# Performance work log

Measured on AMD Instinct MI355X. Metric: run time of the kernel, lower is better.

The kernel has to match this reference:

```python
import jax, jax.numpy as jnp
import numpy as np

N = 8192          # num atoms
K = 32            # neighbors per atom (init kwarg k)
CUTOFF = 10.0     # init kwarg cutoff
NUM_MOLS = 128


def setup_inputs() -> dict:
    key = jax.random.key(0)
    k1, k2 = jax.random.split(key)
    pos = jax.random.normal(k1, (N, 3), dtype=jnp.float32)
    batch = jnp.sort(jax.random.randint(k2, (N,), 0, NUM_MOLS)).astype(jnp.int32)
    return {"pos": pos, "batch": batch}


def _pairwise_dist(pos):
    # ||x_i - x_j|| via the gram-matrix expansion; avoids an [N,N,3] intermediate.
    sq_norm = jnp.sum(pos * pos, axis=-1)                     # [N]
    sq = sq_norm[:, None] + sq_norm[None, :] - 2.0 * (pos @ pos.T)  # [N,N]
    sq = jnp.maximum(sq, 0.0)
    # safe sqrt: exact 0 on the diagonal without nan-producing sqrt'(0) in grads
    safe = jnp.where(sq > 0, sq, 1.0)
    return jnp.where(sq > 0, jnp.sqrt(safe), 0.0)


def reference(pos, batch):
    n = pos.shape[0]
    pdist = _pairwise_dist(pos)                               # [N,N]
    rows = jnp.arange(n)
    diag = rows[:, None] == rows[None, :]
    cross = batch[:, None] != batch[None, :]
    outer = pdist > CUTOFF
    mask = diag | cross | outer
    pdist = jnp.where(mask, CUTOFF, pdist)
    neg_w, indices = jax.lax.top_k(-pdist, K)                 # [N,K] each
    rows_e = jnp.broadcast_to(rows[:, None], indices.shape)
    edge_index = jnp.stack([indices.reshape(-1), rows_e.reshape(-1)])  # [2, N*K]
    edge_weight = -neg_w.reshape(-1)                          # [N*K]
    return edge_index, edge_weight
```

## Files before the change

### kernel.cpp

```cpp
#include <hip/hip_runtime.h>


#define CUTOFF_F 10.0f
#define ROWS_PER_BLOCK 4

__device__ __forceinline__ float readlane_f(float v, int lane) {
    return __int_as_float(__builtin_amdgcn_readlane(__float_as_int(v), lane));
}
__device__ __forceinline__ int readlane_i(int v, int lane) {
    return __builtin_amdgcn_readlane(v, lane);
}
__device__ __forceinline__ unsigned long long shfl_xor_u64(unsigned long long x, int m) {
    const int lo = __shfl_xor((int)(unsigned)(x & 0xffffffffull), m, 64);
    const int hi = __shfl_xor((int)(unsigned)(x >> 32), m, 64);
    return ((unsigned long long)(unsigned)hi << 32) | (unsigned)lo;
}

__device__ __forceinline__ float dist_v(float4 pr, float4 pc, bool diag) {
    if (diag) return CUTOFF_F;
    float dot = __fadd_rn(__fadd_rn(__fmul_rn(pr.x, pc.x), __fmul_rn(pr.y, pc.y)),
                          __fmul_rn(pr.z, pc.z));
    float sq = __fsub_rn(__fadd_rn(pr.w, pc.w), __fadd_rn(dot, dot));
    sq = fmaxf(sq, 0.0f);
    float d = (sq > 0.0f) ? __fsqrt_rn(sq) : 0.0f;
    return (d > CUTOFF_F) ? CUTOFF_F : d;
}

__device__ __forceinline__ float4 load_pos4(const float* __restrict__ pos, int g) {
    float x = pos[g * 3 + 0];
    float y = pos[g * 3 + 1];
    float z = pos[g * 3 + 2];
    float sq = __fadd_rn(__fadd_rn(__fmul_rn(x, x), __fmul_rn(y, y)), __fmul_rn(z, z));
    return make_float4(x, y, z, sq);
}

__device__ __forceinline__ unsigned long long pack_key(float v, int c) {
    return ((unsigned long long)(unsigned)__float_as_int(v) << 32) | (unsigned)c;
}

__device__ __forceinline__ unsigned long long bitonic64(unsigned long long key, int lane) {
#pragma unroll
    for (int k = 2; k <= 64; k <<= 1) {
#pragma unroll
        for (int j = k >> 1; j > 0; j >>= 1) {
            const unsigned long long pk = shfl_xor_u64(key, j);
            const bool take_min = (((lane & j) == 0) == ((lane & k) == 0));
            key = ((pk < key) == take_min) ? pk : key;
        }
    }
    return key;
}

__device__ __forceinline__ void bitonic128(unsigned long long& ka,
                                           unsigned long long& kb, int lane) {
#pragma unroll
    for (int k = 2; k <= 128; k <<= 1) {
#pragma unroll
        for (int j = k >> 1; j > 0; j >>= 1) {
            if (j == 64) {
                const bool alt = ka < kb;
                const unsigned long long mn = alt ? ka : kb;
                const unsigned long long mx = alt ? kb : ka;
                ka = mn; kb = mx;
            } else {
                const unsigned long long pa = shfl_xor_u64(ka, j);
                const unsigned long long pb = shfl_xor_u64(kb, j);
                const bool low = ((lane & j) == 0);
                const bool upA = ((lane & k) == 0);
                const bool upB = (k == 64) ? false : upA;
                ka = ((pa < ka) == (low == upA)) ? pa : ka;
                kb = ((pb < kb) == (low == upB)) ? pb : kb;
            }
        }
    }
}

template <int NCH>
__device__ __forceinline__ void do_fill(const float* v, int m, int K, int lane,
                                        int start, int end, int n, int r, int NK,
                                        float* __restrict__ out) {
    const int mm = n - m;
    for (int fb = 0; fb < K - m; fb += 64) {
        const int t = fb + lane;
        const bool active = t < (K - m);
        int idx = 0;
        bool found = false;
        if (active) {
            if (t < start)            { idx = t;                      found = true; }
            else if (t - start >= mm) { idx = end + (t - start - mm); found = true; }
        }
        if (__any(active && !found)) {
            int cnt = 0;
#pragma unroll
            for (int jj = 0; jj < NCH; ++jj) {
                const int base = 64 * jj;
                const int lim  = min(n - base, 64);
                for (int cc = 0; cc < lim; ++cc) {
                    if (readlane_f(v[jj], cc) == CUTOFF_F) {
                        if (active && !found && cnt == t - start) {
                            idx = start + base + cc; found = true;
                        }
                        ++cnt;
                    }
                }
            }
        }
        if (active) {
            const int o = r * K + m + t;
            out[o]          = (float)idx;
            out[2 * NK + o] = CUTOFF_F;
        }
    }
}

__device__ __forceinline__ void row_core_sort64(const float* __restrict__ pos,
                                                float4 pr, int n, int lane,
                                                int start, int end, int r,
                                                float* __restrict__ out,
                                                int NK, int K) {
    const int c = lane;
    float v[1];
    v[0] = (c < n) ? dist_v(pr, load_pos4(pos, start + c), (start + c) == r)
                   : CUTOFF_F;
    unsigned long long key = pack_key(v[0], c);
    key = bitonic64(key, lane);

    const float vs = __int_as_float((int)(unsigned)(key >> 32));
    const int   cs = (int)(unsigned)(key & 0xffffffffull);
    if (lane < K && vs < CUTOFF_F) {
        const int o = r * K + lane;
        out[o]          = (float)(start + cs);
        out[2 * NK + o] = vs;
    }
    for (int k2 = lane; k2 < K; k2 += 64)
        out[NK + r * K + k2] = (float)r;
    const int m = __popcll(__ballot(v[0] < CUTOFF_F));
    if (m < K) do_fill<1>(v, m, K, lane, start, end, n, r, NK, out);
}

__device__ __forceinline__ void row_core_sort128(const float* __restrict__ pos,
                                                 float4 pr, int n, int lane,
                                                 int start, int end, int r,
                                                 float* __restrict__ out,
                                                 int NK, int K) {
    const int cA = lane, cB = 64 + lane;
    float v[2];
    v[0] = (cA < n) ? dist_v(pr, load_pos4(pos, start + cA), (start + cA) == r)
                    : CUTOFF_F;
    v[1] = (cB < n) ? dist_v(pr, load_pos4(pos, start + cB), (start + cB) == r)
                    : CUTOFF_F;
    unsigned long long ka = pack_key(v[0], cA);
    unsigned long long kb = pack_key(v[1], cB);
    bitonic128(ka, kb, lane);

    const float vsa = __int_as_float((int)(unsigned)(ka >> 32));
    const int   csa = (int)(unsigned)(ka & 0xffffffffull);
    if (lane < K && vsa < CUTOFF_F) {
        const int o = r * K + lane;
        out[o]          = (float)(start + csa);
        out[2 * NK + o] = vsa;
    }
    if (64 + lane < K) {
        const float vsb = __int_as_float((int)(unsigned)(kb >> 32));
        const int   csb = (int)(unsigned)(kb & 0xffffffffull);
        if (vsb < CUTOFF_F) {
            const int o = r * K + 64 + lane;
            out[o]          = (float)(start + csb);
            out[2 * NK + o] = vsb;
        }
    }
    for (int k2 = lane; k2 < K; k2 += 64)
        out[NK + r * K + k2] = (float)r;
    const int m = __popcll(__ballot(v[0] < CUTOFF_F))
                + __popcll(__ballot(v[1] < CUTOFF_F));
    if (m < K) do_fill<2>(v, m, K, lane, start, end, n, r, NK, out);
}

__device__ __attribute__((noinline))
int lower_bound_cold(const int* __restrict__ batch, int lo, int hi, int key) {
    while (lo < hi) {
        int mid = (lo + hi) >> 1;
        if (batch[mid] < key) lo = mid + 1; else hi = mid;
    }
    return lo;
}

__device__ __attribute__((noinline))
void row_core_fallback(const float* __restrict__ pos, float4 pr, int n, int lane,
                       int start, int end, int r, float* __restrict__ out,
                       int NK, int K) {
    int m = 0;
    for (int cb = 0; cb < n; cb += 64) {
        const int c = cb + lane;
        const float v = (c < n)
            ? dist_v(pr, load_pos4(pos, start + c), (start + c) == r) : CUTOFF_F;
        int rk = 0;
        for (int cc = 0; cc < n; ++cc) {
            const float vv = dist_v(pr, load_pos4(pos, start + cc), (start + cc) == r);
            rk += (vv < v) || (vv == v && cc < c);
        }
        if (c < n && v < CUTOFF_F && rk < K) {
            const int o = r * K + rk;
            out[o]          = (float)(start + c);
            out[2 * NK + o] = v;
        }
        m += __popcll(__ballot(c < n && v < CUTOFF_F));
    }
    for (int k2 = lane; k2 < K; k2 += 64)
        out[NK + r * K + k2] = (float)r;
    if (m < K) {
        const int mm = n - m;
        for (int fb = 0; fb < K - m; fb += 64) {
            const int t = fb + lane;
            const bool active = t < (K - m);
            int idx = 0; bool found = false;
            if (active) {
                if (t < start)            { idx = t;                      found = true; }
                else if (t - start >= mm) { idx = end + (t - start - mm); found = true; }
            }
            if (__any(active && !found)) {
                int cnt = 0;
                for (int cc = 0; cc < n; ++cc) {
                    if (dist_v(pr, load_pos4(pos, start + cc), (start + cc) == r)
                        == CUTOFF_F) {
                        if (active && !found && cnt == t - start) {
                            idx = start + cc; found = true;
                        }
                        ++cnt;
                    }
                }
            }
            if (active) {
                const int o = r * K + m + t;
                out[o]          = (float)idx;
                out[2 * NK + o] = CUTOFF_F;
            }
        }
    }
}

__global__ __launch_bounds__(256, 8)
void knn_fused_kernel(const float* __restrict__ pos,
                      const int* __restrict__ batch,
                      float* __restrict__ out,
                      int N, int K) {
    const int w    = threadIdx.x >> 6;
    const int lane = threadIdx.x & 63;
    const int r    = blockIdx.x * ROWS_PER_BLOCK + w;
    if (r >= N) return;
    const int NK = N * K;

    const int iu = r - 63 + lane;
    const int id = r + 1 + lane;
    const int au = batch[max(iu, 0)];
    const int ad = batch[min(id, N - 1)];
    const float4 pr = load_pos4(pos, r);

    const int b = readlane_i(au, 63);

    const unsigned long long mu = __ballot(iu >= 0 && au == b);
    int start;
    if (mu != ~0ull) {
        start = r - __builtin_clzll(~mu) + 1;
    } else {
        const int iu2 = r - 127 + lane;
        const unsigned long long mu2 =
            __ballot(iu2 >= 0 && batch[max(iu2, 0)] == b);
        if (mu2 != ~0ull)           start = r - 63 - __builtin_clzll(~mu2);
        else if (r - 127 <= 0)      start = 0;
        else                        start = lower_bound_cold(batch, 0, r, b);
    }

    const unsigned long long md = __ballot(id < N && ad == b);
    int end;
    if (md != ~0ull) {
        end = r + 1 + __builtin_ctzll(~md);
    } else {
        const int id2 = r + 65 + lane;
        const unsigned long long md2 =
            __ballot(id2 < N && batch[min(id2, N - 1)] == b);
        if (md2 != ~0ull)           end = r + 65 + __builtin_ctzll(~md2);
        else if (r + 129 >= N)      end = N;
        else                        end = lower_bound_cold(batch, r + 1, N, b + 1);
    }

    const int n = end - start;

    if      (n <= 64)  row_core_sort64 (pos, pr, n, lane, start, end, r, out, NK, K);
    else if (n <= 128) row_core_sort128(pos, pr, n, lane, start, end, r, out, NK, K);
    else               row_core_fallback(pos, pr, n, lane, start, end, r, out, NK, K);
}

extern "C" void kernel_launch(void* const* d_in, const int* in_sizes, int n_in,
                              void* d_out, int out_size, void* d_ws, size_t ws_size,
                              hipStream_t stream) {
    const float* pos   = (const float*)d_in[0];
    const int*   batch = (const int*)d_in[1];
    float*       out   = (float*)d_out;

    const int N = in_sizes[1];
    const int K = out_size / (3 * N);

    const int grid = (N + ROWS_PER_BLOCK - 1) / ROWS_PER_BLOCK;
    knn_fused_kernel<<<grid, 256, 0, stream>>>(pos, batch, out, N, K);
}
```

Baseline: 64.96 us.

## Process four rows per wave, sharing column loads and interleaving bitonic sorts

Each wave now handles four consecutive rows instead of one. When all four rows belong to the same molecule, the column positions are loaded once and the row positions are taken by readlane from registers. The four bitonic sorts run interleaved so their shuffles can overlap, which raises ILP and cuts redundant global loads and segment-boundary searches. Rows that straddle a molecule boundary fall back to per-row processing. Register pressure goes up and the launch bound drops to 4 blocks per CU, with 4x fewer waves in flight overall.

Measured after the change: 73.16 us. +12.6%, slower.

```diff
diff --git a/kernel.cpp b/kernel.cpp
--- a/kernel.cpp
+++ b/kernel.cpp
@@ -2,7 +2,9 @@
 
 
 #define CUTOFF_F 10.0f
-#define ROWS_PER_BLOCK 4
+#define ROWS_PER_WAVE 4
+#define WAVES_PER_BLOCK 4
+#define ROWS_PER_BLOCK (ROWS_PER_WAVE * WAVES_PER_BLOCK)
 
 __device__ __forceinline__ float readlane_f(float v, int lane) {
     return __int_as_float(__builtin_amdgcn_readlane(__float_as_int(v), lane));
@@ -38,38 +40,52 @@
     return ((unsigned long long)(unsigned)__float_as_int(v) << 32) | (unsigned)c;
 }
 
-__device__ __forceinline__ unsigned long long bitonic64(unsigned long long key, int lane) {
+template <int R>
+__device__ __forceinline__ void bitonic64xR(unsigned long long* key, int lane) {
 #pragma unroll
     for (int k = 2; k <= 64; k <<= 1) {
 #pragma unroll
         for (int j = k >> 1; j > 0; j >>= 1) {
-            const unsigned long long pk = shfl_xor_u64(key, j);
             const bool take_min = (((lane & j) == 0) == ((lane & k) == 0));
-            key = ((pk < key) == take_min) ? pk : key;
-        }
-    }
-    return key;
-}
-
-__device__ __forceinline__ void bitonic128(unsigned long long& ka,
-                                           unsigned long long& kb, int lane) {
+            unsigned long long pk[R];
+#pragma unroll
+            for (int t = 0; t < R; ++t) pk[t] = shfl_xor_u64(key[t], j);
+#pragma unroll
+            for (int t = 0; t < R; ++t)
+                key[t] = ((pk[t] < key[t]) == take_min) ? pk[t] : key[t];
+        }
+    }
+}
+
+template <int R>
+__device__ __forceinline__ void bitonic128xR(unsigned long long* ka,
+                                             unsigned long long* kb, int lane) {
 #pragma unroll
     for (int k = 2; k <= 128; k <<= 1) {
 #pragma unroll
         for (int j = k >> 1; j > 0; j >>= 1) {
             if (j == 64) {
-                const bool alt = ka < kb;
-                const unsigned long long mn = alt ? ka : kb;
-                const unsigned long long mx = alt ? kb : ka;
-                ka = mn; kb = mx;
+#pragma unroll
+                for (int t = 0; t < R; ++t) {
+                    const bool alt = ka[t] < kb[t];
+                    const unsigned long long mn = alt ? ka[t] : kb[t];
+                    const unsigned long long mx = alt ? kb[t] : ka[t];
+                    ka[t] = mn; kb[t] = mx;
+                }
             } else {
-                const unsigned long long pa = shfl_xor_u64(ka, j);
-                const unsigned long long pb = shfl_xor_u64(kb, j);
                 const bool low = ((lane & j) == 0);
                 const bool upA = ((lane & k) == 0);
                 const bool upB = (k == 64) ? false : upA;
-                ka = ((pa < ka) == (low == upA)) ? pa : ka;
-                kb = ((pb < kb) == (low == upB)) ? pb : kb;
+                unsigned long long pa[R], pb[R];
+#pragma unroll
+                for (int t = 0; t < R; ++t) pa[t] = shfl_xor_u64(ka[t], j);
+#pragma unroll
+                for (int t = 0; t < R; ++t) pb[t] = shfl_xor_u64(kb[t], j);
+#pragma unroll
+                for (int t = 0; t < R; ++t) {
+                    ka[t] = ((pa[t] < ka[t]) == (low == upA)) ? pa[t] : ka[t];
+                    kb[t] = ((pb[t] < kb[t]) == (low == upB)) ? pb[t] : kb[t];
+                }
             }
         }
     }
@@ -113,20 +129,27 @@
     }
 }
 
-__device__ __forceinline__ void row_core_sort64(const float* __restrict__ pos,
-                                                float4 pr, int n, int lane,
-                                                int start, int end, int r,
-                                                float* __restrict__ out,
-                                                int NK, int K) {
+__device__ __attribute__((noinline))
+int lower_bound_cold(const int* __restrict__ batch, int lo, int hi, int key) {
+    while (lo < hi) {
+        int mid = (lo + hi) >> 1;
+        if (batch[mid] < key) lo = mid + 1; else hi = mid;
+    }
+    return lo;
+}
+
+__device__ __attribute__((noinline))
+void row_core_sort64(const float* __restrict__ pos, float4 pr, int n, int lane,
+                     int start, int end, int r, float* __restrict__ out,
+                     int NK, int K) {
     const int c = lane;
     float v[1];
     v[0] = (c < n) ? dist_v(pr, load_pos4(pos, start + c), (start + c) == r)
                    : CUTOFF_F;
-    unsigned long long key = pack_key(v[0], c);
-    key = bitonic64(key, lane);
-
-    const float vs = __int_as_float((int)(unsigned)(key >> 32));
-    const int   cs = (int)(unsigned)(key & 0xffffffffull);
+    unsigned long long key[1] = { pack_key(v[0], c) };
+    bitonic64xR<1>(key, lane);
+    const float vs = __int_as_float((int)(unsigned)(key[0] >> 32));
+    const int   cs = (int)(unsigned)(key[0] & 0xffffffffull);
     if (lane < K && vs < CUTOFF_F) {
         const int o = r * K + lane;
         out[o]          = (float)(start + cs);
@@ -138,31 +161,29 @@
     if (m < K) do_fill<1>(v, m, K, lane, start, end, n, r, NK, out);
 }
 
-__device__ __forceinline__ void row_core_sort128(const float* __restrict__ pos,
-                                                 float4 pr, int n, int lane,
-                                                 int start, int end, int r,
-                                                 float* __restrict__ out,
-                                                 int NK, int K) {
+__device__ __attribute__((noinline))
+void row_core_sort128(const float* __restrict__ pos, float4 pr, int n, int lane,
+                      int start, int end, int r, float* __restrict__ out,
+                      int NK, int K) {
     const int cA = lane, cB = 64 + lane;
     float v[2];
     v[0] = (cA < n) ? dist_v(pr, load_pos4(pos, start + cA), (start + cA) == r)
                     : CUTOFF_F;
     v[1] = (cB < n) ? dist_v(pr, load_pos4(pos, start + cB), (start + cB) == r)
                     : CUTOFF_F;
-    unsigned long long ka = pack_key(v[0], cA);
-    unsigned long long kb = pack_key(v[1], cB);
-    bitonic128(ka, kb, lane);
-
-    const float vsa = __int_as_float((int)(unsigned)(ka >> 32));
-    const int   csa = (int)(unsigned)(ka & 0xffffffffull);
+    unsigned long long ka[1] = { pack_key(v[0], cA) };
+    unsigned long long kb[1] = { pack_key(v[1], cB) };
+    bitonic128xR<1>(ka, kb, lane);
+    const float vsa = __int_as_float((int)(unsigned)(ka[0] >> 32));
+    const int   csa = (int)(unsigned)(ka[0] & 0xffffffffull);
     if (lane < K && vsa < CUTOFF_F) {
         const int o = r * K + lane;
         out[o]          = (float)(start + csa);
         out[2 * NK + o] = vsa;
     }
     if (64 + lane < K) {
-        const float vsb = __int_as_float((int)(unsigned)(kb >> 32));
-        const int   csb = (int)(unsigned)(kb & 0xffffffffull);
+        const float vsb = __int_as_float((int)(unsigned)(kb[0] >> 32));
+        const int   csb = (int)(unsigned)(kb[0] & 0xffffffffull);
         if (vsb < CUTOFF_F) {
             const int o = r * K + 64 + lane;
             out[o]          = (float)(start + csb);
@@ -174,15 +195,6 @@
     const int m = __popcll(__ballot(v[0] < CUTOFF_F))
                 + __popcll(__ballot(v[1] < CUTOFF_F));
     if (m < K) do_fill<2>(v, m, K, lane, start, end, n, r, NK, out);
-}
-
-__device__ __attribute__((noinline))
-int lower_bound_cold(const int* __restrict__ batch, int lo, int hi, int key) {
-    while (lo < hi) {
-        int mid = (lo + hi) >> 1;
-        if (batch[mid] < key) lo = mid + 1; else hi = mid;
-    }
-    return lo;
 }
 
 __device__ __attribute__((noinline))
@@ -239,56 +251,164 @@
     }
 }
 
-__global__ __launch_bounds__(256, 8)
-void knn_fused_kernel(const float* __restrict__ pos,
-                      const int* __restrict__ batch,
-                      float* __restrict__ out,
-                      int N, int K) {
+__global__ __launch_bounds__(256, 4)
+void knn_quad_kernel(const float* __restrict__ pos,
+                     const int* __restrict__ batch,
+                     float* __restrict__ out,
+                     int N, int K) {
     const int w    = threadIdx.x >> 6;
     const int lane = threadIdx.x & 63;
-    const int r    = blockIdx.x * ROWS_PER_BLOCK + w;
-    if (r >= N) return;
+    const int r0   = (blockIdx.x * WAVES_PER_BLOCK + w) * ROWS_PER_WAVE;
+    if (r0 >= N) return;
     const int NK = N * K;
 
-    const int iu = r - 63 + lane;
-    const int id = r + 1 + lane;
+    const int iu = r0 - 63 + lane;
+    const int id = r0 + 1 + lane;
     const int au = batch[max(iu, 0)];
     const int ad = batch[min(id, N - 1)];
-    const float4 pr = load_pos4(pos, r);
-
-    const int b = readlane_i(au, 63);
-
-    const unsigned long long mu = __ballot(iu >= 0 && au == b);
-    int start;
-    if (mu != ~0ull) {
-        start = r - __builtin_clzll(~mu) + 1;
+    const int b0 = readlane_i(au, 63);
+
+    const bool same = (r0 + ROWS_PER_WAVE - 1 < N) &&
+                      (readlane_i(ad, ROWS_PER_WAVE - 2) == b0);
+
+    if (same) {
+        const unsigned long long Mu = __ballot(iu >= 0 && au == b0);
+        const unsigned long long Md = __ballot(id < N  && ad == b0);
+        int start, end;
+        if (~Mu == 0ull) start = lower_bound_cold(batch, 0, r0, b0);
+        else             start = r0 - (__builtin_clzll(~Mu) - 1);
+        if (~Md == 0ull) end   = lower_bound_cold(batch, r0 + 1, N, b0 + 1);
+        else             end   = r0 + 1 + __builtin_ctzll(~Md);
+        const int n  = end - start;
+        const int d0 = r0 - start;
+
+        if (n <= 64) {
+            const int c = lane;
+            const int g = start + min(c, n - 1);
+            const float x = pos[g * 3 + 0];
+            const float y = pos[g * 3 + 1];
+            const float z = pos[g * 3 + 2];
+            const float sq = __fadd_rn(__fadd_rn(__fmul_rn(x, x), __fmul_rn(y, y)),
+                                       __fmul_rn(z, z));
+            const bool cval = (c < n);
+            unsigned long long key[ROWS_PER_WAVE];
+            float vrow[ROWS_PER_WAVE];
+#pragma unroll
+            for (int i = 0; i < ROWS_PER_WAVE; ++i) {
+                const int d = d0 + i;
+                const float4 pr = make_float4(readlane_f(x, d), readlane_f(y, d),
+                                              readlane_f(z, d), readlane_f(sq, d));
+                const float4 pc = make_float4(x, y, z, sq);
+                const float v = (cval && c != d) ? dist_v(pr, pc, false) : CUTOFF_F;
+                vrow[i] = v;
+                key[i]  = pack_key(v, c);
+            }
+            bitonic64xR<ROWS_PER_WAVE>(key, lane);
+#pragma unroll
+            for (int i = 0; i < ROWS_PER_WAVE; ++i) {
+                const int r = r0 + i;
+                const float vs = __int_as_float((int)(unsigned)(key[i] >> 32));
+                const int   cs = (int)(unsigned)(key[i] & 0xffffffffull);
+                if (lane < K && vs < CUTOFF_F) {
+                    const int o = r * K + lane;
+                    out[o]          = (float)(start + cs);
+                    out[2 * NK + o] = vs;
+                }
+                for (int k2 = lane; k2 < K; k2 += 64)
+                    out[NK + r * K + k2] = (float)r;
+                const int m = __popcll(__ballot(vrow[i] < CUTOFF_F));
+                if (m < K) do_fill<1>(&vrow[i], m, K, lane, start, end, n, r, NK, out);
+            }
+        } else if (n <= 128) {
+            const int cA = lane, cB = 64 + lane;
+            const int gA = start + min(cA, n - 1);
+            const int gB = start + min(cB, n - 1);
+            const float xa = pos[gA * 3 + 0], ya = pos[gA * 3 + 1], za = pos[gA * 3 + 2];
+            const float xb = pos[gB * 3 + 0], yb = pos[gB * 3 + 1], zb = pos[gB * 3 + 2];
+            const float sqa = __fadd_rn(__fadd_rn(__fmul_rn(xa, xa), __fmul_rn(ya, ya)),
+                                        __fmul_rn(za, za));
+            const float sqb = __fadd_rn(__fadd_rn(__fmul_rn(xb, xb), __fmul_rn(yb, yb)),
+                                        __fmul_rn(zb, zb));
+            const bool aval = (cA < n), bval = (cB < n);
+            unsigned long long ka[ROWS_PER_WAVE], kb[ROWS_PER_WAVE];
+            float va[ROWS_PER_WAVE], vb[ROWS_PER_WAVE];
+#pragma unroll
+            for (int i = 0; i < ROWS_PER_WAVE; ++i) {
+                const int d = d0 + i;
+                float4 pr;
+                if (d < 64) pr = make_float4(readlane_f(xa, d), readlane_f(ya, d),
+                                             readlane_f(za, d), readlane_f(sqa, d));
+                else        pr = make_float4(readlane_f(xb, d - 64), readlane_f(yb, d - 64),
+                                             readlane_f(zb, d - 64), readlane_f(sqb, d - 64));
+                const float fa = (aval && cA != d)
+                    ? dist_v(pr, make_float4(xa, ya, za, sqa), false) : CUTOFF_F;
+                const float fb = (bval && cB != d)
+                    ? dist_v(pr, make_float4(xb, yb, zb, sqb), false) : CUTOFF_F;
+                va[i] = fa; vb[i] = fb;
+                ka[i] = pack_key(fa, cA);
+                kb[i] = pack_key(fb, cB);
+            }
+            bitonic128xR<ROWS_PER_WAVE>(ka, kb, lane);
+#pragma unroll
+            for (int i = 0; i < ROWS_PER_WAVE; ++i) {
+                const int r = r0 + i;
+                const float vsa = __int_as_float((int)(unsigned)(ka[i] >> 32));
+                const int   csa = (int)(unsigned)(ka[i] & 0xffffffffull);
+                if (lane < K && vsa < CUTOFF_F) {
+                    const int o = r * K + lane;
+                    out[o]          = (float)(start + csa);
+                    out[2 * NK + o] = vsa;
+                }
+                if (64 + lane < K) {
+                    const float vsb = __int_as_float((int)(unsigned)(kb[i] >> 32));
+                    const int   csb = (int)(unsigned)(kb[i] & 0xffffffffull);
+                    if (vsb < CUTOFF_F) {
+                        const int o = r * K + 64 + lane;
+                        out[o]          = (float)(start + csb);
+                        out[2 * NK + o] = vsb;
+                    }
+                }
+                for (int k2 = lane; k2 < K; k2 += 64)
+                    out[NK + r * K + k2] = (float)r;
+                const int m = __popcll(__ballot(va[i] < CUTOFF_F))
+                            + __popcll(__ballot(vb[i] < CUTOFF_F));
+                if (m < K) {
+                    float v2[2] = { va[i], vb[i] };
+                    do_fill<2>(v2, m, K, lane, start, end, n, r, NK, out);
+                }
+            }
+        } else {
+#pragma unroll
+            for (int i = 0; i < ROWS_PER_WAVE; ++i) {
+                const int r = r0 + i;
+                row_core_fallback(pos, load_pos4(pos, r), n, lane, start, end, r,
+                                  out, NK, K);
+            }
+        }
     } else {
-        const int iu2 = r - 127 + lane;
-        const unsigned long long mu2 =
-            __ballot(iu2 >= 0 && batch[max(iu2, 0)] == b);
-        if (mu2 != ~0ull)           start = r - 63 - __builtin_clzll(~mu2);
-        else if (r - 127 <= 0)      start = 0;
-        else                        start = lower_bound_cold(batch, 0, r, b);
-    }
-
-    const unsigned long long md = __ballot(id < N && ad == b);
-    int end;
-    if (md != ~0ull) {
-        end = r + 1 + __builtin_ctzll(~md);
-    } else {
-        const int id2 = r + 65 + lane;
-        const unsigned long long md2 =
-            __ballot(id2 < N && batch[min(id2, N - 1)] == b);
-        if (md2 != ~0ull)           end = r + 65 + __builtin_ctzll(~md2);
-        else if (r + 129 >= N)      end = N;
-        else                        end = lower_bound_cold(batch, r + 1, N, b + 1);
-    }
-
-    const int n = end - start;
-
-    if      (n <= 64)  row_core_sort64 (pos, pr, n, lane, start, end, r, out, NK, K);
-    else if (n <= 128) row_core_sort128(pos, pr, n, lane, start, end, r, out, NK, K);
-    else               row_core_fallback(pos, pr, n, lane, start, end, r, out, NK, K);
+#pragma unroll
+        for (int i = 0; i < ROWS_PER_WAVE; ++i) {
+            const int r = r0 + i;
+            if (r >= N) break;
+            const int b = (i == 0) ? b0 : readlane_i(ad, i - 1);
+            const unsigned long long Mu = __ballot(iu >= 0 && au == b);
+            const unsigned long long Md = __ballot(id < N  && ad == b);
+            const unsigned long long X =
+                (i == 0) ? Mu : ((Mu >> i) | (Md << (64 - i)));
+            int start, end;
+            if (~X == 0ull) start = lower_bound_cold(batch, 0, r, b);
+            else            start = r - (__builtin_clzll(~X) - 1);
+            const unsigned long long Y = Md >> i;
+            const int T = (~Y == 0ull) ? 64 : __builtin_ctzll(~Y);
+            if (T >= 64 - i) end = lower_bound_cold(batch, r + 1, N, b + 1);
+            else             end = r + 1 + T;
+            const int n = end - start;
+            const float4 pr = load_pos4(pos, r);
+            if      (n <= 64)  row_core_sort64 (pos, pr, n, lane, start, end, r, out, NK, K);
+            else if (n <= 128) row_core_sort128(pos, pr, n, lane, start, end, r, out, NK, K);
+            else               row_core_fallback(pos, pr, n, lane, start, end, r, out, NK, K);
+        }
+    }
 }
 
 extern "C" void kernel_launch(void* const* d_in, const int* in_sizes, int n_in,
@@ -302,5 +422,5 @@
     const int K = out_size / (3 * N);
 
     const int grid = (N + ROWS_PER_BLOCK - 1) / ROWS_PER_BLOCK;
-    knn_fused_kernel<<<grid, 256, 0, stream>>>(pos, batch, out, N, K);
-}
+    knn_quad_kernel<<<grid, 256, 0, stream>>>(pos, batch, out, N, K);
+}
```

## Sort 32-bit truncated keys with DPP shuffles and recover exact distances via bpermute

Applied to the files above, without the earlier changes.

Replaces the 64-bit (distance, index) sort keys with 32-bit keys: the distance bits are truncated to free the low 7 bits for the column index. This halves the cross-lane shuffle traffic in the bitonic networks, and DPP is used for the j=1, 2 and 8 stages. Exact distances are then fetched with ds_bpermute, and the row's own position is read from the column data with readlane instead of a separate load. The risk is that truncating the key can reorder distances that differ only in their low mantissa bits, or break ties differently from the reference top_k.

Result: faster. 59.90 us (-7.8%).

```diff
diff --git a/kernel.cpp b/kernel.cpp
--- a/kernel.cpp
+++ b/kernel.cpp
@@ -3,6 +3,7 @@
 
 #define CUTOFF_F 10.0f
 #define ROWS_PER_BLOCK 4
+#define KEY_TRUNC 0xFFFFFF80u
 
 __device__ __forceinline__ float readlane_f(float v, int lane) {
     return __int_as_float(__builtin_amdgcn_readlane(__float_as_int(v), lane));
@@ -10,10 +11,19 @@
 __device__ __forceinline__ int readlane_i(int v, int lane) {
     return __builtin_amdgcn_readlane(v, lane);
 }
-__device__ __forceinline__ unsigned long long shfl_xor_u64(unsigned long long x, int m) {
-    const int lo = __shfl_xor((int)(unsigned)(x & 0xffffffffull), m, 64);
-    const int hi = __shfl_xor((int)(unsigned)(x >> 32), m, 64);
-    return ((unsigned long long)(unsigned)hi << 32) | (unsigned)lo;
+__device__ __forceinline__ float bperm_f(float v, int srclane) {
+    return __int_as_float(__builtin_amdgcn_ds_bpermute(srclane << 2, __float_as_int(v)));
+}
+
+template <int CTRL>
+__device__ __forceinline__ unsigned dpp_u32(unsigned x) {
+    return (unsigned)__builtin_amdgcn_update_dpp((int)x, (int)x, CTRL, 0xf, 0xf, true);
+}
+__device__ __forceinline__ unsigned stage_shfl32(unsigned x, int j) {
+    if (j == 1) return dpp_u32<0xB1>(x);
+    if (j == 2) return dpp_u32<0x4E>(x);
+    if (j == 8) return dpp_u32<0x128>(x);
+    return (unsigned)__shfl_xor((int)x, j, 64);
 }
 
 __device__ __forceinline__ float dist_v(float4 pr, float4 pc, bool diag) {
@@ -34,16 +44,12 @@
     return make_float4(x, y, z, sq);
 }
 
-__device__ __forceinline__ unsigned long long pack_key(float v, int c) {
-    return ((unsigned long long)(unsigned)__float_as_int(v) << 32) | (unsigned)c;
-}
-
-__device__ __forceinline__ unsigned long long bitonic64(unsigned long long key, int lane) {
+__device__ __forceinline__ unsigned bitonic64_u32(unsigned key, int lane) {
 #pragma unroll
     for (int k = 2; k <= 64; k <<= 1) {
 #pragma unroll
         for (int j = k >> 1; j > 0; j >>= 1) {
-            const unsigned long long pk = shfl_xor_u64(key, j);
+            const unsigned pk = stage_shfl32(key, j);
             const bool take_min = (((lane & j) == 0) == ((lane & k) == 0));
             key = ((pk < key) == take_min) ? pk : key;
         }
@@ -51,20 +57,18 @@
     return key;
 }
 
-__device__ __forceinline__ void bitonic128(unsigned long long& ka,
-                                           unsigned long long& kb, int lane) {
+__device__ __forceinline__ void bitonic128_u32(unsigned& ka, unsigned& kb, int lane) {
 #pragma unroll
     for (int k = 2; k <= 128; k <<= 1) {
 #pragma unroll
         for (int j = k >> 1; j > 0; j >>= 1) {
             if (j == 64) {
-                const bool alt = ka < kb;
-                const unsigned long long mn = alt ? ka : kb;
-                const unsigned long long mx = alt ? kb : ka;
+                const unsigned mn = min(ka, kb);
+                const unsigned mx = max(ka, kb);
                 ka = mn; kb = mx;
             } else {
-                const unsigned long long pa = shfl_xor_u64(ka, j);
-                const unsigned long long pb = shfl_xor_u64(kb, j);
+                const unsigned pa = stage_shfl32(ka, j);
+                const unsigned pb = stage_shfl32(kb, j);
                 const bool low = ((lane & j) == 0);
                 const bool upA = ((lane & k) == 0);
                 const bool upB = (k == 64) ? false : upA;
@@ -114,23 +118,33 @@
 }
 
 __device__ __forceinline__ void row_core_sort64(const float* __restrict__ pos,
-                                                float4 pr, int n, int lane,
+                                                int n, int lane,
                                                 int start, int end, int r,
                                                 float* __restrict__ out,
                                                 int NK, int K) {
     const int c = lane;
+    const int d = r - start;
+    const int g = start + min(c, n - 1);
+    const float x = pos[g * 3 + 0];
+    const float y = pos[g * 3 + 1];
+    const float z = pos[g * 3 + 2];
+    const float sq = __fadd_rn(__fadd_rn(__fmul_rn(x, x), __fmul_rn(y, y)),
+                               __fmul_rn(z, z));
+    const float4 pc = make_float4(x, y, z, sq);
+    const float4 pr = make_float4(readlane_f(x, d), readlane_f(y, d),
+                                  readlane_f(z, d), readlane_f(sq, d));
     float v[1];
-    v[0] = (c < n) ? dist_v(pr, load_pos4(pos, start + c), (start + c) == r)
-                   : CUTOFF_F;
-    unsigned long long key = pack_key(v[0], c);
-    key = bitonic64(key, lane);
-
-    const float vs = __int_as_float((int)(unsigned)(key >> 32));
-    const int   cs = (int)(unsigned)(key & 0xffffffffull);
-    if (lane < K && vs < CUTOFF_F) {
+    v[0] = (c < n && c != d) ? dist_v(pr, pc, false) : CUTOFF_F;
+
+    unsigned key = (((unsigned)__float_as_int(v[0])) & KEY_TRUNC) | (unsigned)c;
+    key = bitonic64_u32(key, lane);
+
+    const int   cs = (int)(key & 0x7Fu);
+    const float vx = bperm_f(v[0], cs);
+    if (lane < K && vx < CUTOFF_F) {
         const int o = r * K + lane;
         out[o]          = (float)(start + cs);
-        out[2 * NK + o] = vs;
+        out[2 * NK + o] = vx;
     }
     for (int k2 = lane; k2 < K; k2 += 64)
         out[NK + r * K + k2] = (float)r;
@@ -139,34 +153,53 @@
 }
 
 __device__ __forceinline__ void row_core_sort128(const float* __restrict__ pos,
-                                                 float4 pr, int n, int lane,
+                                                 int n, int lane,
                                                  int start, int end, int r,
                                                  float* __restrict__ out,
                                                  int NK, int K) {
     const int cA = lane, cB = 64 + lane;
+    const int d  = r - start;
+    const int gA = start + min(cA, n - 1);
+    const int gB = start + min(cB, n - 1);
+    const float xa = pos[gA * 3 + 0], ya = pos[gA * 3 + 1], za = pos[gA * 3 + 2];
+    const float xb = pos[gB * 3 + 0], yb = pos[gB * 3 + 1], zb = pos[gB * 3 + 2];
+    const float sqa = __fadd_rn(__fadd_rn(__fmul_rn(xa, xa), __fmul_rn(ya, ya)),
+                                __fmul_rn(za, za));
+    const float sqb = __fadd_rn(__fadd_rn(__fmul_rn(xb, xb), __fmul_rn(yb, yb)),
+                                __fmul_rn(zb, zb));
+    float4 pr;
+    if (d < 64) pr = make_float4(readlane_f(xa, d), readlane_f(ya, d),
+                                 readlane_f(za, d), readlane_f(sqa, d));
+    else        pr = make_float4(readlane_f(xb, d - 64), readlane_f(yb, d - 64),
+                                 readlane_f(zb, d - 64), readlane_f(sqb, d - 64));
     float v[2];
-    v[0] = (cA < n) ? dist_v(pr, load_pos4(pos, start + cA), (start + cA) == r)
-                    : CUTOFF_F;
-    v[1] = (cB < n) ? dist_v(pr, load_pos4(pos, start + cB), (start + cB) == r)
-                    : CUTOFF_F;
-    unsigned long long ka = pack_key(v[0], cA);
-    unsigned long long kb = pack_key(v[1], cB);
-    bitonic128(ka, kb, lane);
-
-    const float vsa = __int_as_float((int)(unsigned)(ka >> 32));
-    const int   csa = (int)(unsigned)(ka & 0xffffffffull);
-    if (lane < K && vsa < CUTOFF_F) {
+    v[0] = (cA < n && cA != d) ? dist_v(pr, make_float4(xa, ya, za, sqa), false)
+                               : CUTOFF_F;
+    v[1] = (cB < n && cB != d) ? dist_v(pr, make_float4(xb, yb, zb, sqb), false)
+                               : CUTOFF_F;
+
+    unsigned ka = (((unsigned)__float_as_int(v[0])) & KEY_TRUNC) | (unsigned)cA;
+    unsigned kb = (((unsigned)__float_as_int(v[1])) & KEY_TRUNC) | (unsigned)cB;
+    bitonic128_u32(ka, kb, lane);
+
+    const int   csa = (int)(ka & 0x7Fu);
+    const float g0  = bperm_f(v[0], csa & 63);
+    const float g1  = bperm_f(v[1], csa & 63);
+    const float vxa = (csa < 64) ? g0 : g1;
+    if (lane < K && vxa < CUTOFF_F) {
         const int o = r * K + lane;
         out[o]          = (float)(start + csa);
-        out[2 * NK + o] = vsa;
+        out[2 * NK + o] = vxa;
     }
     if (64 + lane < K) {
-        const float vsb = __int_as_float((int)(unsigned)(kb >> 32));
-        const int   csb = (int)(unsigned)(kb & 0xffffffffull);
-        if (vsb < CUTOFF_F) {
+        const int   csb = (int)(kb & 0x7Fu);
+        const float h0  = bperm_f(v[0], csb & 63);
+        const float h1  = bperm_f(v[1], csb & 63);
+        const float vxb = (csb < 64) ? h0 : h1;
+        if (vxb < CUTOFF_F) {
             const int o = r * K + 64 + lane;
             out[o]          = (float)(start + csb);
-            out[2 * NK + o] = vsb;
+            out[2 * NK + o] = vxb;
         }
     }
     for (int k2 = lane; k2 < K; k2 += 64)
@@ -254,7 +287,6 @@
     const int id = r + 1 + lane;
     const int au = batch[max(iu, 0)];
     const int ad = batch[min(id, N - 1)];
-    const float4 pr = load_pos4(pos, r);
 
     const int b = readlane_i(au, 63);
 
@@ -286,9 +318,10 @@
 
     const int n = end - start;
 
-    if      (n <= 64)  row_core_sort64 (pos, pr, n, lane, start, end, r, out, NK, K);
-    else if (n <= 128) row_core_sort128(pos, pr, n, lane, start, end, r, out, NK, K);
-    else               row_core_fallback(pos, pr, n, lane, start, end, r, out, NK, K);
+    if      (n <= 64)  row_core_sort64 (pos, n, lane, start, end, r, out, NK, K);
+    else if (n <= 128) row_core_sort128(pos, n, lane, start, end, r, out, NK, K);
+    else               row_core_fallback(pos, load_pos4(pos, r), n, lane, start,
+                                         end, r, out, NK, K);
 }
 
 extern "C" void kernel_launch(void* const* d_in, const int* in_sizes, int n_in,
```
